# Performance work log

Hardware: AMD Instinct MI355X
Metric: run time of the kernel (lower is better)

The kernel has to match this reference:

```python
import jax, jax.numpy as jnp
import numpy as np

LMAX, MMAX = 4, 2
C_IN, C_OUT = 128, 128           # sphere_channels, m_output_channels
NUM_EXPERTS = 8
NUM_SYSTEMS = 16
NUM_EDGES = 12288
M_SIZE = [LMAX + 1, 2 * (LMAX - 1 + 1), 2 * (LMAX - 2 + 1)]  # [5, 8, 6]


def _mole_linear(x, W, ce, b=None):
    """MoLE linear: per-edge expert mixing of weights, equivalently mixing of
    per-expert outputs.  x: [N, in] or [N, 2, in]; W: [K, in, out]; ce: [N, K]."""
    if x.ndim == 2:
        z = jnp.einsum('ni,kio->nko', x, W)        # [N, K, out]
        y = jnp.einsum('nk,nko->no', ce, z)
    else:
        z = jnp.einsum('nci,kio->nkco', x, W)      # [N, K, 2, out]
        y = jnp.einsum('nk,nkco->nco', ce, z)
    if b is not None:
        y = y + ce @ b                              # mixed bias, b: [K, out]
    return y


def setup_inputs() -> dict:
    key = jax.random.key(0)
    ks = jax.random.split(key, 8)
    num_mcoef = sum(M_SIZE)  # 19
    x = jax.random.normal(ks[0], (NUM_EDGES, num_mcoef, C_IN), dtype=jnp.float32)
    x_edge = jax.random.normal(ks[1], (NUM_EDGES, C_IN), dtype=jnp.float32)
    expert_coefficients = jax.random.uniform(ks[2], (NUM_SYSTEMS, NUM_EXPERTS), dtype=jnp.float32)
    edge_batch = jax.random.randint(ks[3], (NUM_EDGES,), 0, NUM_SYSTEMS)
    # fc_m0: in = (lmax+1)*C, out = (lmax+1)*C_out, with bias
    in0 = (LMAX + 1) * C_IN
    out0 = (LMAX + 1) * C_OUT
    W_m0 = jax.random.normal(ks[4], (NUM_EXPERTS, in0, out0), dtype=jnp.float32) * 0.02
    b_m0 = jnp.zeros((NUM_EXPERTS, out0), dtype=jnp.float32)
    # so2_m_conv m: in = (lmax-m+1)*C, out = 2*(lmax-m+1)*C_out, no bias
    nc1 = LMAX - 1 + 1
    W_m1 = jax.random.normal(ks[5], (NUM_EXPERTS, nc1 * C_IN, 2 * nc1 * C_OUT), dtype=jnp.float32) * 0.02
    nc2 = LMAX - 2 + 1
    W_m2 = jax.random.normal(ks[6], (NUM_EXPERTS, nc2 * C_IN, 2 * nc2 * C_OUT), dtype=jnp.float32) * 0.02
    return {
        'x': x, 'x_edge': x_edge,
        'expert_coefficients': expert_coefficients, 'edge_batch': edge_batch,
        'W_m0': W_m0, 'b_m0': b_m0, 'W_m1': W_m1, 'W_m2': W_m2,
    }


def reference(x, x_edge, expert_coefficients, edge_batch, W_m0, b_m0, W_m1, W_m2):
    N = x.shape[0]
    ce = expert_coefficients[edge_batch]               # [N, K] per-edge mix coeffs
    x0, x1, x2 = jnp.split(x, np.cumsum(M_SIZE[:-1]), axis=1)
    # m = 0 branch (internal_weights=True -> no radial rescale)
    y0 = _mole_linear(x0.reshape(N, -1), W_m0, ce, b_m0)
    out = [y0.reshape(N, -1, C_OUT)]                   # [N, lmax+1, C_out]
    # m >= 1 branches: SO(2) real/imag recombination
    for m, Wm, xm in ((1, W_m1, x1), (2, W_m2, x2)):
        nc = LMAX - m + 1
        xm = xm.reshape(N, 2, nc * C_IN)
        ym = _mole_linear(xm, Wm, ce)                  # [N, 2, 2*nc*C_out]
        ym = ym.reshape(N, 4, nc * C_OUT)
        x_m_r = ym[:, 0] - ym[:, 3]                    # x_r_0 - x_i_1
        x_m_i = ym[:, 2] + ym[:, 1]                    # x_r_1 + x_i_0
        out.append(x_m_r.reshape(N, nc, C_OUT))
        out.append(x_m_i.reshape(N, nc, C_OUT))
    return jnp.concatenate(out, axis=1)                # [N, 19, C_out]
```

## Files before the change

### kernel.cpp

```cpp
#include <hip/hip_runtime.h>
#include <cstdint>

#define N_EDGES 12288
#define ROWLEN  2432
#define CAP     2048

typedef __bf16 bf16;
typedef __bf16 bf16x8 __attribute__((ext_vector_type(8)));
typedef __bf16 bf16x4 __attribute__((ext_vector_type(4)));
typedef float  f32x4  __attribute__((ext_vector_type(4)));

#define ELEMS0 (640*640)
#define ELEMS1 (1024*1024)
#define ELEMS2 (768*768)

#define WS_IDX_OFF   1024
#define WS_BIAS_OFF  (WS_IDX_OFF + 16*CAP*4)
#define WS_W_OFF     (WS_BIAS_OFF + 16*640*4)
#define WZ_ELEMS     ((size_t)16*(ELEMS0+ELEMS1+ELEMS2))

template<int B> struct Cfg;
template<> struct Cfg<0> { static constexpr int K=640,  KS=640, XOFF=0,    NT=5;
                           static constexpr size_t WOFF=0; };
template<> struct Cfg<1> { static constexpr int K=1024, KS=512, XOFF=640,  NT=8;
                           static constexpr size_t WOFF=(size_t)16*ELEMS0; };
template<> struct Cfg<2> { static constexpr int K=768,  KS=384, XOFF=1664, NT=6;
                           static constexpr size_t WOFF=(size_t)16*ELEMS0+(size_t)16*ELEMS1; };

__device__ __forceinline__ void async_copy16(const void* g, void* l) {
  auto gp = reinterpret_cast<const __attribute__((address_space(1))) unsigned int*>(
      reinterpret_cast<uintptr_t>(g));
  auto lp = reinterpret_cast<__attribute__((address_space(3))) unsigned int*>(
      (unsigned int)reinterpret_cast<uintptr_t>(l));
  __builtin_amdgcn_global_load_lds(gp, lp, 16, 0, 0);
}

__global__ void bucket_kernel(const int* __restrict__ eb, int* __restrict__ counts,
                              int* __restrict__ idxb) {
  __shared__ int hcnt[16], hbase[16];
  int tid = threadIdx.x;
  int t = blockIdx.x * 256 + tid;
  if (tid < 16) hcnt[tid] = 0;
  __syncthreads();
  int s = -1, lp = 0;
  if (t < N_EDGES) { s = eb[t]; lp = atomicAdd(&hcnt[s], 1); }
  __syncthreads();
  if (tid < 16) hbase[tid] = atomicAdd(counts + tid, hcnt[tid]);
  __syncthreads();
  if (s >= 0) { int p = hbase[s] + lp; if (p < CAP) idxb[s * CAP + p] = t; }
}

__global__ void bias_kernel(const float* __restrict__ ce, const float* __restrict__ b0,
                            float* __restrict__ bias) {
  int t = blockIdx.x * 256 + threadIdx.x;
  int s = t / 640, c = t - s * 640;
  float a = 0.f;
#pragma unroll
  for (int e = 0; e < 8; ++e) a += ce[s * 8 + e] * b0[e * 640 + c];
  bias[t] = a;
}

template<int B>
__device__ __forceinline__ void mix_body(const float* __restrict__ Wsrc,
                                         const float* ce_s,
                                         unsigned short* __restrict__ Wz, int pos) {
  constexpr int N = Cfg<B>::K, KS = Cfg<B>::KS, NT = N / 128, HALF = N / 2;
  constexpr int SRC_STRIDE = KS * N;
  constexpr size_t DST_STRIDE = (size_t)Cfg<B>::K * N;
  int nn = pos & 127, kgrp = (pos >> 7) & 3, rest = pos >> 9;
  int nt = rest % NT, kblk = rest / NT;
  int i0 = kblk * 32 + kgrp * 8;
  int c  = nt * 128 + nn;
  int si = i0, sc = c; float sg = 1.f;
  if (B > 0 && i0 >= KS) {
    si = i0 - KS;
    if (c < HALF) { sc = c + HALF; sg = -1.f; } else { sc = c - HALF; }
  }
  float w[8][8];
  const float* p0 = Wsrc + (size_t)si * N + sc;
#pragma unroll
  for (int e = 0; e < 8; ++e) {
    const float* p = p0 + (size_t)e * SRC_STRIDE;
#pragma unroll
    for (int j = 0; j < 8; ++j)
      w[e][j] = sg * p[(size_t)j * N];
  }
  unsigned short* db = Wz + Cfg<B>::WOFF + (size_t)pos * 8;
#pragma unroll
  for (int s = 0; s < 16; ++s) {
    float a[8] = {0, 0, 0, 0, 0, 0, 0, 0};
#pragma unroll
    for (int e = 0; e < 8; ++e) {
      float cc = ce_s[s * 8 + e];
#pragma unroll
      for (int j = 0; j < 8; ++j) a[j] += cc * w[e][j];
    }
    bf16x8 v;
#pragma unroll
    for (int j = 0; j < 8; ++j) v[j] = (bf16)a[j];
    *(bf16x8*)(db + s * DST_STRIDE) = v;
  }
}

__global__ __launch_bounds__(256) void mix_all(const float* __restrict__ W0,
                                               const float* __restrict__ W1,
                                               const float* __restrict__ W2,
                                               const float* __restrict__ ce,
                                               unsigned short* __restrict__ Wz) {
  __shared__ float ce_s[128];
  int tid = threadIdx.x;
  if (tid < 128) ce_s[tid] = ce[tid];
  __syncthreads();
  int bx = blockIdx.x;
  if (bx < 200)      mix_body<0>(W0, ce_s, Wz, bx * 256 + tid);
  else if (bx < 712) mix_body<1>(W1, ce_s, Wz, (bx - 200) * 256 + tid);
  else               mix_body<2>(W2, ce_s, Wz, (bx - 712) * 256 + tid);
}

template<int B>
__device__ __forceinline__ void gemm_body(
    const float* __restrict__ x, const char* __restrict__ zeros,
    const unsigned short* __restrict__ Wz,
    const int* __restrict__ counts, const int* __restrict__ idxb,
    const float* __restrict__ bias, float* __restrict__ out,
    int s, int mt, int nt2, char* sm, int* eidx)
{
  constexpr int K = Cfg<B>::K, NT = Cfg<B>::NT, KB = K / 32, XOFF = Cfg<B>::XOFF;
  int cnt = counts[s];
  int m0 = mt * 128;
  if (m0 >= cnt) return;
  int tid = threadIdx.x;
  if (tid < 128) eidx[tid] = (m0 + tid < cnt) ? idxb[s * CAP + m0 + tid] : -1;
  __syncthreads();
  char* Acur = sm;          char* Anxt = sm + 8192;
  char* Bc = sm + 16384;    char* Bm = sm + 32768;    char* Bn = sm + 49152;
  int wv = tid >> 6, ln = tid & 63;
  int wm = wv >> 1, wn = wv & 1;
  int kq = ln >> 4, lm = ln & 15;
  int c0 = nt2 * 2;
  int c16 = tid & 7, rbase = tid >> 3;
  int kq_w = c16 >> 1, half = c16 & 1;
  const char* arow4[4]; int kinc4[4];
#pragma unroll
  for (int i = 0; i < 4; ++i) {
    int e = eidx[rbase + 32 * i];
    if (e >= 0) { arow4[i] = (const char*)(x + (size_t)e * ROWLEN + XOFF); kinc4[i] = 128; }
    else        { arow4[i] = zeros; kinc4[i] = 0; }
  }
  const unsigned short* wb = Wz + Cfg<B>::WOFF + (size_t)s * K * K;

  f32x4 sreg[4];
  auto loadA = [&](int kb) {
#pragma unroll
    for (int i = 0; i < 4; ++i)
      sreg[i] = *(const f32x4*)(arow4[i] + (size_t)kb * kinc4[i] + c16 * 16);
  };
  auto writeA = [&](char* dst) {
#pragma unroll
    for (int i = 0; i < 4; ++i) {
      int r = rbase + 32 * i;
      bf16x4 v;
      v[0] = (bf16)sreg[i][0]; v[1] = (bf16)sreg[i][1];
      v[2] = (bf16)sreg[i][2]; v[3] = (bf16)sreg[i][3];
      *(bf16x4*)(dst + kq_w * 2048 + ((r ^ (kq_w << 1)) * 16) + half * 8) = v;
    }
  };
  auto stageB = [&](int kb, char* dst) {
    const unsigned short* base = wb + (size_t)kb * (NT * 4096);
#pragma unroll
    for (int i = 0; i < 4; ++i) {
      int c = i * 256 + tid;
      int ck = c0 + (c >> 9); if (ck > NT - 1) ck = NT - 1;
      async_copy16(base + (size_t)ck * 4096 + (c & 511) * 8,
                   dst + (i * 256 + wv * 64) * 16);
    }
  };

  f32x4 acc[4][8];
#pragma unroll
  for (int i = 0; i < 4; ++i)
#pragma unroll
    for (int j = 0; j < 8; ++j) {
      acc[i][j][0] = 0.f; acc[i][j][1] = 0.f; acc[i][j][2] = 0.f; acc[i][j][3] = 0.f;
    }

  loadA(0);
  stageB(0, Bc);
  writeA(Acur);
  asm volatile("s_waitcnt vmcnt(0)" ::: "memory");
  stageB(1, Bm);
  loadA(1);
  asm volatile("s_waitcnt lgkmcnt(0)" ::: "memory");
  __builtin_amdgcn_s_barrier();
  __builtin_amdgcn_sched_barrier(0);

#pragma unroll 1
  for (int kb = 0; kb < KB; ++kb) {
    if (kb + 2 < KB) stageB(kb + 2, Bn);
    bf16x8 af[4], bq[8];
#pragma unroll
    for (int mi = 0; mi < 4; ++mi) {
      int r = wm * 64 + mi * 16 + lm;
      af[mi] = *(const bf16x8*)(Acur + kq * 2048 + ((r ^ (kq << 1)) * 16));
    }
#pragma unroll
    for (int ni = 0; ni < 8; ++ni)
      bq[ni] = *(const bf16x8*)(Bc + wn * 8192 + kq * 2048 + (ni * 16 + lm) * 16);
    __builtin_amdgcn_s_setprio(1);
#pragma unroll
    for (int mi = 0; mi < 4; ++mi)
#pragma unroll
      for (int ni = 0; ni < 8; ++ni)
        acc[mi][ni] = __builtin_amdgcn_mfma_f32_16x16x32_bf16(af[mi], bq[ni], acc[mi][ni], 0, 0, 0);
    __builtin_amdgcn_s_setprio(0);
    if (kb + 1 < KB) {
      writeA(Anxt);
      if (kb + 2 < KB) loadA(kb + 2);
    }
    asm volatile("s_waitcnt lgkmcnt(0)" ::: "memory");
    __builtin_amdgcn_s_barrier();
    __builtin_amdgcn_sched_barrier(0);
    char* t = Acur; Acur = Anxt; Anxt = t;
    char* tb = Bc; Bc = Bm; Bm = Bn; Bn = tb;
  }
  int cc = c0 + wn;
  if (cc >= NT) return;
  float bv[8] = {0, 0, 0, 0, 0, 0, 0, 0};
  if (B == 0) {
#pragma unroll
    for (int ni = 0; ni < 8; ++ni)
      bv[ni] = bias[s * 640 + cc * 128 + ni * 16 + lm];
  }
#pragma unroll
  for (int mi = 0; mi < 4; ++mi) {
#pragma unroll
    for (int r = 0; r < 4; ++r) {
      int row = wm * 64 + mi * 16 + kq * 4 + r;
      int e = eidx[row];
      if (e < 0) continue;
      float* po = out + (size_t)e * ROWLEN + XOFF + cc * 128 + lm;
#pragma unroll
      for (int ni = 0; ni < 8; ++ni) po[ni * 16] = acc[mi][ni][r] + bv[ni];
    }
  }
}

__global__ __launch_bounds__(256, 2) void gemm_all(
    const float* __restrict__ x, const char* __restrict__ zeros,
    const unsigned short* __restrict__ Wz,
    const int* __restrict__ counts, const int* __restrict__ idxb,
    const float* __restrict__ bias, float* __restrict__ out) {
  extern __shared__ char sm[];
  __shared__ int eidx[128];
  int g = blockIdx.x;
  int xcd = g & 7, j = g >> 3;
  int s = xcd + 8 * (j / 160);
  int r = j % 160;
  int mt = r / 10, bx = r % 10;
  if (bx < 3)      gemm_body<0>(x, zeros, Wz, counts, idxb, bias, out, s, mt, bx,     sm, eidx);
  else if (bx < 7) gemm_body<1>(x, zeros, Wz, counts, idxb, bias, out, s, mt, bx - 3, sm, eidx);
  else             gemm_body<2>(x, zeros, Wz, counts, idxb, bias, out, s, mt, bx - 7, sm, eidx);
}

extern "C" void kernel_launch(void* const* d_in, const int* in_sizes, int n_in,
                              void* d_out, int out_size, void* d_ws, size_t ws_size,
                              hipStream_t stream) {
  const float* x  = (const float*)d_in[0];
  const float* ce = (const float*)d_in[2];
  const int*   eb = (const int*)d_in[3];
  const float* W0 = (const float*)d_in[4];
  const float* b0 = (const float*)d_in[5];
  const float* W1 = (const float*)d_in[6];
  const float* W2 = (const float*)d_in[7];
  float* out = (float*)d_out;
  char* ws = (char*)d_ws;
  int*   counts = (int*)ws;
  char*  zeros  = ws + 256;
  int*   idxb   = (int*)(ws + WS_IDX_OFF);
  float* bias   = (float*)(ws + WS_BIAS_OFF);
  unsigned short* Wz = (unsigned short*)(ws + WS_W_OFF);

  hipMemsetAsync(ws, 0, 1024, stream);
  bucket_kernel<<<48, 256, 0, stream>>>(eb, counts, idxb);
  bias_kernel<<<40, 256, 0, stream>>>(ce, b0, bias);
  mix_all<<<1000, 256, 0, stream>>>(W0, W1, W2, ce, Wz);
  gemm_all<<<2560, 256, 65536, stream>>>(x, zeros, Wz, counts, idxb, bias, out);
}
```

Before: 325.0 us.

## Merge prep kernels into one launch and double-buffer A registers in GEMM loop

The bucket, bias and weight-mixing kernels are combined into a single prep launch with block-range dispatch, removing two kernel launches and their serialization gaps. In the GEMM main loop, the A-tile global loads are now issued two k-steps ahead into alternating register sets, alongside the B async copy, via a 2x-unrolled loop. This gives the A loads a full iteration of latency hiding instead of being issued right before the barrier. The cost is extra VGPR pressure from a second set of four f32x4 registers, which could lower occupancy. The initial vmcnt wait was also removed, which relies on the compiler inserting the waits needed before the first A write.

```diff
diff --git a/kernel.cpp b/kernel.cpp
--- a/kernel.cpp
+++ b/kernel.cpp
@@ -33,31 +33,6 @@
   auto lp = reinterpret_cast<__attribute__((address_space(3))) unsigned int*>(
       (unsigned int)reinterpret_cast<uintptr_t>(l));
   __builtin_amdgcn_global_load_lds(gp, lp, 16, 0, 0);
-}
-
-__global__ void bucket_kernel(const int* __restrict__ eb, int* __restrict__ counts,
-                              int* __restrict__ idxb) {
-  __shared__ int hcnt[16], hbase[16];
-  int tid = threadIdx.x;
-  int t = blockIdx.x * 256 + tid;
-  if (tid < 16) hcnt[tid] = 0;
-  __syncthreads();
-  int s = -1, lp = 0;
-  if (t < N_EDGES) { s = eb[t]; lp = atomicAdd(&hcnt[s], 1); }
-  __syncthreads();
-  if (tid < 16) hbase[tid] = atomicAdd(counts + tid, hcnt[tid]);
-  __syncthreads();
-  if (s >= 0) { int p = hbase[s] + lp; if (p < CAP) idxb[s * CAP + p] = t; }
-}
-
-__global__ void bias_kernel(const float* __restrict__ ce, const float* __restrict__ b0,
-                            float* __restrict__ bias) {
-  int t = blockIdx.x * 256 + threadIdx.x;
-  int s = t / 640, c = t - s * 640;
-  float a = 0.f;
-#pragma unroll
-  for (int e = 0; e < 8; ++e) a += ce[s * 8 + e] * b0[e * 640 + c];
-  bias[t] = a;
 }
 
 template<int B>
@@ -102,19 +77,40 @@
   }
 }
 
-__global__ __launch_bounds__(256) void mix_all(const float* __restrict__ W0,
-                                               const float* __restrict__ W1,
-                                               const float* __restrict__ W2,
-                                               const float* __restrict__ ce,
-                                               unsigned short* __restrict__ Wz) {
+__global__ __launch_bounds__(256) void prep_all(
+    const float* __restrict__ W0, const float* __restrict__ W1,
+    const float* __restrict__ W2, const float* __restrict__ ce,
+    unsigned short* __restrict__ Wz,
+    const int* __restrict__ eb, int* __restrict__ counts, int* __restrict__ idxb,
+    const float* __restrict__ b0, float* __restrict__ bias) {
   __shared__ float ce_s[128];
+  __shared__ int hcnt[16], hbase[16];
   int tid = threadIdx.x;
-  if (tid < 128) ce_s[tid] = ce[tid];
-  __syncthreads();
   int bx = blockIdx.x;
-  if (bx < 200)      mix_body<0>(W0, ce_s, Wz, bx * 256 + tid);
-  else if (bx < 712) mix_body<1>(W1, ce_s, Wz, (bx - 200) * 256 + tid);
-  else               mix_body<2>(W2, ce_s, Wz, (bx - 712) * 256 + tid);
+  if (bx < 1000) {
+    if (tid < 128) ce_s[tid] = ce[tid];
+    __syncthreads();
+    if (bx < 200)      mix_body<0>(W0, ce_s, Wz, bx * 256 + tid);
+    else if (bx < 712) mix_body<1>(W1, ce_s, Wz, (bx - 200) * 256 + tid);
+    else               mix_body<2>(W2, ce_s, Wz, (bx - 712) * 256 + tid);
+  } else if (bx < 1048) {
+    int t = (bx - 1000) * 256 + tid;
+    if (tid < 16) hcnt[tid] = 0;
+    __syncthreads();
+    int s = -1, lp = 0;
+    if (t < N_EDGES) { s = eb[t]; lp = atomicAdd(&hcnt[s], 1); }
+    __syncthreads();
+    if (tid < 16) hbase[tid] = atomicAdd(counts + tid, hcnt[tid]);
+    __syncthreads();
+    if (s >= 0) { int p = hbase[s] + lp; if (p < CAP) idxb[s * CAP + p] = t; }
+  } else {
+    int t = (bx - 1048) * 256 + tid;
+    int s = t / 640, c = t - s * 640;
+    float a = 0.f;
+#pragma unroll
+    for (int e = 0; e < 8; ++e) a += ce[s * 8 + e] * b0[e * 640 + c];
+    bias[t] = a;
+  }
 }
 
 template<int B>
@@ -126,6 +122,7 @@
     int s, int mt, int nt2, char* sm, int* eidx)
 {
   constexpr int K = Cfg<B>::K, NT = Cfg<B>::NT, KB = K / 32, XOFF = Cfg<B>::XOFF;
+  static_assert((K / 32) % 2 == 0, "KB must be even for the 2x-unrolled loop");
   int cnt = counts[s];
   int m0 = mt * 128;
   if (m0 >= cnt) return;
@@ -149,23 +146,26 @@
   }
   const unsigned short* wb = Wz + Cfg<B>::WOFF + (size_t)s * K * K;
 
-  f32x4 sreg[4];
-  auto loadA = [&](int kb) {
-#pragma unroll
-    for (int i = 0; i < 4; ++i)
-      sreg[i] = *(const f32x4*)(arow4[i] + (size_t)kb * kinc4[i] + c16 * 16);
-  };
-  auto writeA = [&](char* dst) {
+  auto loadA2 = [&](int kb, f32x4& r0, f32x4& r1, f32x4& r2, f32x4& r3)
+      __attribute__((always_inline)) {
+    r0 = *(const f32x4*)(arow4[0] + (size_t)kb * kinc4[0] + c16 * 16);
+    r1 = *(const f32x4*)(arow4[1] + (size_t)kb * kinc4[1] + c16 * 16);
+    r2 = *(const f32x4*)(arow4[2] + (size_t)kb * kinc4[2] + c16 * 16);
+    r3 = *(const f32x4*)(arow4[3] + (size_t)kb * kinc4[3] + c16 * 16);
+  };
+  auto writeA2 = [&](char* dst, f32x4& r0, f32x4& r1, f32x4& r2, f32x4& r3)
+      __attribute__((always_inline)) {
+    f32x4 rr[4] = {r0, r1, r2, r3};
 #pragma unroll
     for (int i = 0; i < 4; ++i) {
       int r = rbase + 32 * i;
       bf16x4 v;
-      v[0] = (bf16)sreg[i][0]; v[1] = (bf16)sreg[i][1];
-      v[2] = (bf16)sreg[i][2]; v[3] = (bf16)sreg[i][3];
+      v[0] = (bf16)rr[i][0]; v[1] = (bf16)rr[i][1];
+      v[2] = (bf16)rr[i][2]; v[3] = (bf16)rr[i][3];
       *(bf16x4*)(dst + kq_w * 2048 + ((r ^ (kq_w << 1)) * 16) + half * 8) = v;
     }
   };
-  auto stageB = [&](int kb, char* dst) {
+  auto stageB = [&](int kb, char* dst) __attribute__((always_inline)) {
     const unsigned short* base = wb + (size_t)kb * (NT * 4096);
 #pragma unroll
     for (int i = 0; i < 4; ++i) {
@@ -184,44 +184,53 @@
       acc[i][j][0] = 0.f; acc[i][j][1] = 0.f; acc[i][j][2] = 0.f; acc[i][j][3] = 0.f;
     }
 
-  loadA(0);
+  auto kstep = [&](int kb, f32x4& o0, f32x4& o1, f32x4& o2, f32x4& o3,
+                           f32x4& n0, f32x4& n1, f32x4& n2, f32x4& n3)
+      __attribute__((always_inline)) {
+    if (kb + 2 < KB) {
+      stageB(kb + 2, Bn);
+      loadA2(kb + 2, n0, n1, n2, n3);
+    }
+    __builtin_amdgcn_sched_barrier(0);
+    bf16x8 af[4], bq[8];
+#pragma unroll
+    for (int mi = 0; mi < 4; ++mi) {
+      int r = wm * 64 + mi * 16 + lm;
+      af[mi] = *(const bf16x8*)(Acur + kq * 2048 + ((r ^ (kq << 1)) * 16));
+    }
+#pragma unroll
+    for (int ni = 0; ni < 8; ++ni)
+      bq[ni] = *(const bf16x8*)(Bc + wn * 8192 + kq * 2048 + (ni * 16 + lm) * 16);
+    __builtin_amdgcn_s_setprio(1);
+#pragma unroll
+    for (int mi = 0; mi < 4; ++mi)
+#pragma unroll
+      for (int ni = 0; ni < 8; ++ni)
+        acc[mi][ni] = __builtin_amdgcn_mfma_f32_16x16x32_bf16(af[mi], bq[ni], acc[mi][ni], 0, 0, 0);
+    __builtin_amdgcn_s_setprio(0);
+    if (kb + 1 < KB)
+      writeA2(Anxt, o0, o1, o2, o3);
+    asm volatile("s_waitcnt lgkmcnt(0)" ::: "memory");
+    __builtin_amdgcn_s_barrier();
+    __builtin_amdgcn_sched_barrier(0);
+    { char* t = Acur; Acur = Anxt; Anxt = t; }
+    { char* tb = Bc; Bc = Bm; Bm = Bn; Bn = tb; }
+  };
+
+  f32x4 a0, a1, a2, a3, b0, b1, b2, b3;
   stageB(0, Bc);
-  writeA(Acur);
-  asm volatile("s_waitcnt vmcnt(0)" ::: "memory");
+  loadA2(0, a0, a1, a2, a3);
+  writeA2(Acur, a0, a1, a2, a3);
   stageB(1, Bm);
-  loadA(1);
+  loadA2(1, a0, a1, a2, a3);
   asm volatile("s_waitcnt lgkmcnt(0)" ::: "memory");
   __builtin_amdgcn_s_barrier();
   __builtin_amdgcn_sched_barrier(0);
 
 #pragma unroll 1
-  for (int kb = 0; kb < KB; ++kb) {
-    if (kb + 2 < KB) stageB(kb + 2, Bn);
-    bf16x8 af[4], bq[8];
-#pragma unroll
-    for (int mi = 0; mi < 4; ++mi) {
-      int r = wm * 64 + mi * 16 + lm;
-      af[mi] = *(const bf16x8*)(Acur + kq * 2048 + ((r ^ (kq << 1)) * 16));
-    }
-#pragma unroll
-    for (int ni = 0; ni < 8; ++ni)
-      bq[ni] = *(const bf16x8*)(Bc + wn * 8192 + kq * 2048 + (ni * 16 + lm) * 16);
-    __builtin_amdgcn_s_setprio(1);
-#pragma unroll
-    for (int mi = 0; mi < 4; ++mi)
-#pragma unroll
-      for (int ni = 0; ni < 8; ++ni)
-        acc[mi][ni] = __builtin_amdgcn_mfma_f32_16x16x32_bf16(af[mi], bq[ni], acc[mi][ni], 0, 0, 0);
-    __builtin_amdgcn_s_setprio(0);
-    if (kb + 1 < KB) {
-      writeA(Anxt);
-      if (kb + 2 < KB) loadA(kb + 2);
-    }
-    asm volatile("s_waitcnt lgkmcnt(0)" ::: "memory");
-    __builtin_amdgcn_s_barrier();
-    __builtin_amdgcn_sched_barrier(0);
-    char* t = Acur; Acur = Anxt; Anxt = t;
-    char* tb = Bc; Bc = Bm; Bm = Bn; Bn = tb;
+  for (int kb = 0; kb < KB; kb += 2) {
+    kstep(kb,     a0, a1, a2, a3,  b0, b1, b2, b3);
+    kstep(kb + 1, b0, b1, b2, b3,  a0, a1, a2, a3);
   }
   int cc = c0 + wn;
   if (cc >= NT) return;
@@ -281,8 +290,6 @@
   unsigned short* Wz = (unsigned short*)(ws + WS_W_OFF);
 
   hipMemsetAsync(ws, 0, 1024, stream);
-  bucket_kernel<<<48, 256, 0, stream>>>(eb, counts, idxb);
-  bias_kernel<<<40, 256, 0, stream>>>(ce, b0, bias);
-  mix_all<<<1000, 256, 0, stream>>>(W0, W1, W2, ce, Wz);
+  prep_all<<<1088, 256, 0, stream>>>(W0, W1, W2, ce, Wz, eb, counts, idxb, b0, bias);
   gemm_all<<<2560, 256, 65536, stream>>>(x, zeros, Wz, counts, idxb, bias, out);
 }
```

Result: slower. 352.9 us (+8.6%).
